# Performance work log

Measured on AMD Instinct MI355X. Metric: run time of the kernel, lower is better.

## Reference

```python
import jax, jax.numpy as jnp
import numpy as np
import math

E = 8          # num_experts
IN = 1024      # input_size
HID = 512      # head_size (expert hidden)
TOP_K = 2
B, P = 8, 1024


def setup_inputs() -> dict:
    key = jax.random.key(0)
    k1, k2, k3, k4, k5 = jax.random.split(key, 5)
    # expert weights init like ParallelExperts.reset_parameters (uniform xavier-ish)
    std1 = math.sqrt(2.0 / (IN + HID)); a1 = math.sqrt(3.0) * std1
    std2 = math.sqrt(2.0 / (HID + IN)); a2 = math.sqrt(3.0) * std2
    return {
        "x": jax.random.normal(k1, (B, P, IN), dtype=jnp.float32),
        "Q_isp": jax.random.normal(k2, (B, P, 1, IN), dtype=jnp.float32),
        "K_isp": jax.random.normal(k3, (B, P, E, IN), dtype=jnp.float32),
        "w1": jax.random.uniform(k4, (E, IN, HID), minval=-a1, maxval=a1, dtype=jnp.float32),
        "w2": jax.random.uniform(k5, (E, HID, IN), minval=-a2, maxval=a2, dtype=jnp.float32),
    }


def _gates(Q_isp, K_isp):
    # attention-based gating, eval path (no noise)
    N = K_isp.shape[2]
    scale = 1.0 / math.sqrt(K_isp.shape[-1])
    # [B,P,1,N] -> [T,N]
    scores = jnp.einsum('bpqd,bpnd->bpqn', Q_isp, K_isp)[:, :, 0, :].reshape(-1, N) * scale
    logits = jnp.nan_to_num(scores, nan=0.0, posinf=20.0, neginf=-20.0)
    probs = jax.nn.softmax(logits, axis=1)
    top_g, top_i = jax.lax.top_k(probs, TOP_K)
    # renormalize top-k gates; denominator detached as in torch (.detach())
    top_g = top_g / jax.lax.stop_gradient(top_g.sum(axis=1, keepdims=True) + 1e-6)
    T = probs.shape[0]
    gates = jnp.zeros_like(probs).at[jnp.arange(T)[:, None], top_i].set(top_g)
    return gates  # [T, E]


def reference(x, Q_isp, K_isp, w1, w2):
    gates = _gates(Q_isp, K_isp)                       # [T,E]
    T = gates.shape[0]
    xt = x.reshape(T, -1)                              # [T,IN]
    # grouped expert GEMMs (dense-masked form; gates are 0 off top-k)
    h = jax.nn.gelu(jnp.einsum('ti,eio->teo', xt, w1), approximate=False)  # [T,E,HID]
    y = jnp.einsum('teo,eoi->tei', h, w2)              # [T,E,IN]
    out = jnp.einsum('tei,te->ti', y, gates)           # combine with gates
    return out.reshape(x.shape)
```

## Files before the change

### kernel.cpp

```cpp
#include <hip/hip_runtime.h>
#include <math.h>

#define TT 8192
#define NE 8
#define DIN 1024
#define DH 512

typedef __attribute__((ext_vector_type(8))) short short8;
typedef __attribute__((ext_vector_type(4))) float f32x4;
typedef __attribute__((ext_vector_type(4))) unsigned short us4;

static const size_t OFF_CNT    = 0;
static const size_t OFF_BASE   = 256;
static const size_t OFF_TOKEXP = 512;
static const size_t OFF_GPAIR  = OFF_TOKEXP + (size_t)TT * 8;
static const size_t OFF_SLOT0  = OFF_GPAIR  + (size_t)TT * 8;
static const size_t OFF_SLOT1  = OFF_SLOT0  + (size_t)TT * 4;
static const size_t OFF_TOK    = OFF_SLOT1  + (size_t)TT * 4;
static const size_t OFF_GATE   = OFF_TOK    + (size_t)NE * TT * 4;
static const size_t OFF_XB     = OFF_GATE   + (size_t)NE * TT * 4;
static const size_t OFF_W1T    = OFF_XB     + (size_t)TT * DIN * 2;
static const size_t OFF_W2T    = OFF_W1T    + (size_t)NE * DH * DIN * 2;
static const size_t OFF_H      = OFF_W2T    + (size_t)NE * DIN * DH * 2;
static const size_t OFF_Y      = OFF_H      + (size_t)2 * TT * DH * 2;

__device__ __forceinline__ unsigned short f2bf(float f) {
    union { float f; unsigned u; } v; v.f = f;
    unsigned r = (v.u + 0x7fffu + ((v.u >> 16) & 1u)) >> 16;
    return (unsigned short)r;
}
__device__ __forceinline__ float bf2f(unsigned short u) {
    union { unsigned u; float f; } v; v.u = ((unsigned)u) << 16;
    return v.f;
}
__device__ __forceinline__ void async_copy16(const void* g, void* l) {
    __builtin_amdgcn_global_load_lds(
        (const __attribute__((address_space(1))) void*)g,
        (__attribute__((address_space(3))) void*)l, 16, 0, 0);
}

__global__ __launch_bounds__(256) void convert_x_kernel(const float* __restrict__ x,
                                                        unsigned short* __restrict__ xb)
{
    size_t i = ((size_t)blockIdx.x * 256 + threadIdx.x) * 8;
    float4 a = *reinterpret_cast<const float4*>(x + i);
    float4 b = *reinterpret_cast<const float4*>(x + i + 4);
    us4 o0 = { f2bf(a.x), f2bf(a.y), f2bf(a.z), f2bf(a.w) };
    us4 o1 = { f2bf(b.x), f2bf(b.y), f2bf(b.z), f2bf(b.w) };
    *reinterpret_cast<us4*>(xb + i)     = o0;
    *reinterpret_cast<us4*>(xb + i + 4) = o1;
}

__global__ __launch_bounds__(256) void convert_w_kernel(const float* __restrict__ src,
                                                        unsigned short* __restrict__ dst,
                                                        int K, int N)
{
    int e = blockIdx.z;
    int k0 = blockIdx.x * 32, n0 = blockIdx.y * 32;
    __shared__ float tile[32][33];
    int tx = threadIdx.x & 31, ty = threadIdx.x >> 5;
    const float* s = src + ((size_t)e * K + k0) * N + n0;
#pragma unroll
    for (int r = 0; r < 32; r += 8) tile[ty + r][tx] = s[(size_t)(ty + r) * N + tx];
    __syncthreads();
    unsigned short* d = dst + ((size_t)e * N + n0) * K + k0;
#pragma unroll
    for (int r = 0; r < 32; r += 8) d[(size_t)(ty + r) * K + tx] = f2bf(tile[tx][ty + r]);
}

__global__ __launch_bounds__(256) void gate_kernel(
    const float* __restrict__ Q, const float* __restrict__ Kc,
    int2* __restrict__ tokexp, float2* __restrict__ gpair)
{
    int wave = threadIdx.x >> 6, lane = threadIdx.x & 63;
    int t = blockIdx.x * 4 + wave;
    const float4* q4 = reinterpret_cast<const float4*>(Q + (size_t)t * DIN);
    const float4* k4 = reinterpret_cast<const float4*>(Kc + (size_t)t * NE * DIN);
    float4 q[4];
#pragma unroll
    for (int j = 0; j < 4; ++j) q[j] = q4[j * 64 + lane];
    float part[NE];
#pragma unroll
    for (int e = 0; e < NE; ++e) {
        float s = 0.0f;
#pragma unroll
        for (int j = 0; j < 4; ++j) {
            float4 kv = k4[e * 256 + j * 64 + lane];
            s += q[j].x * kv.x + q[j].y * kv.y + q[j].z * kv.z + q[j].w * kv.w;
        }
        part[e] = s;
    }
#pragma unroll
    for (int e = 0; e < NE; ++e) {
#pragma unroll
        for (int m = 1; m < 64; m <<= 1) part[e] += __shfl_xor(part[e], m);
    }
    if (lane == 0) {
        float s[NE];
#pragma unroll
        for (int e = 0; e < NE; ++e) {
            float v = part[e] * 0.03125f;
            if (isnan(v)) v = 0.0f;
            else if (isinf(v)) v = (v > 0.0f) ? 20.0f : -20.0f;
            s[e] = v;
        }
        float m = s[0];
        for (int e = 1; e < NE; ++e) m = fmaxf(m, s[e]);
        float p[NE]; float sum = 0.0f;
        for (int e = 0; e < NE; ++e) { p[e] = expf(s[e] - m); sum += p[e]; }
        float inv = 1.0f / sum;
        for (int e = 0; e < NE; ++e) p[e] *= inv;
        int i0 = 0;
        for (int e = 1; e < NE; ++e) if (p[e] > p[i0]) i0 = e;
        int i1 = (i0 == 0) ? 1 : 0;
        for (int e = 0; e < NE; ++e) if (e != i0 && p[e] > p[i1]) i1 = e;
        float denom = p[i0] + p[i1] + 1e-6f;
        tokexp[t] = make_int2(i0, i1);
        gpair[t]  = make_float2(p[i0] / denom, p[i1] / denom);
    }
}

__global__ __launch_bounds__(1024) void count_kernel(const int2* __restrict__ tokexp,
                                                     int* __restrict__ cnt)
{
    int e = blockIdx.x;
    int tid = threadIdx.x;
    int local = 0;
#pragma unroll
    for (int r = 0; r < TT / 1024; ++r) {
        int2 te = tokexp[r * 1024 + tid];
        local += (te.x == e || te.y == e) ? 1 : 0;
    }
#pragma unroll
    for (int m = 1; m < 64; m <<= 1) local += __shfl_xor(local, m);
    __shared__ int wsum[16];
    int wave = tid >> 6, lane = tid & 63;
    if (lane == 0) wsum[wave] = local;
    __syncthreads();
    if (tid == 0) {
        int s = 0;
        for (int w = 0; w < 16; ++w) s += wsum[w];
        cnt[e] = s;
    }
}

__global__ void scan_kernel(const int* __restrict__ cnt, int* __restrict__ base)
{
    if (threadIdx.x == 0) {
        int s = 0;
        for (int e = 0; e < NE; ++e) { base[e] = s; s += cnt[e]; }
    }
}

__global__ __launch_bounds__(1024) void build_kernel(
    const int2* __restrict__ tokexp, const float2* __restrict__ gpair,
    const int* __restrict__ base,
    int* __restrict__ tok_list, float* __restrict__ gate_list,
    int* __restrict__ slot0, int* __restrict__ slot1)
{
    int e = blockIdx.x;
    int tid = threadIdx.x;
    int wave = tid >> 6, lane = tid & 63;
    __shared__ int wsum[16];
    __shared__ int running;
    if (tid == 0) running = base[e];
    __syncthreads();
    int eb = base[e];
#pragma unroll 1
    for (int r = 0; r < TT / 1024; ++r) {
        int t = r * 1024 + tid;
        int2 te = tokexp[t];
        float2 g = gpair[t];
        bool f0 = (te.x == e), f1 = (te.y == e);
        bool f = f0 || f1;
        unsigned long long mask = __ballot(f);
        int mypos = __popcll(mask & ((1ull << lane) - 1ull));
        if (lane == 0) wsum[wave] = __popcll(mask);
        __syncthreads();
        int off = 0, total = 0;
        for (int w = 0; w < 16; ++w) {
            int c = wsum[w];
            if (w < wave) off += c;
            total += c;
        }
        int pos = running + off + mypos;
        if (f) {
            int j = pos - eb;
            tok_list[e * TT + j]  = t;
            gate_list[e * TT + j] = f0 ? g.x : g.y;
            if (f0) slot0[t] = pos; else slot1[t] = pos;
        }
        __syncthreads();
        if (tid == 0) running += total;
        __syncthreads();
    }
}

__global__ __launch_bounds__(256) void gemm1_kernel(
    const unsigned short* __restrict__ xb, const unsigned short* __restrict__ w1t,
    const int* __restrict__ cnt, const int* __restrict__ base,
    const int* __restrict__ tok_list, unsigned short* __restrict__ h)
{
    int e = blockIdx.z;
    int Te = cnt[e];
    int m0 = blockIdx.x * 128;
    if (m0 >= Te) return;
    int n0 = blockIdx.y * 128;

    __shared__ __align__(16) char smem[16384];
    __shared__ int rows[128];
    char* As = smem;
    char* Bs = smem + 8192;

    int tid = threadIdx.x;
    if (tid < 128) rows[tid] = (m0 + tid < Te) ? tok_list[e * TT + m0 + tid] : 0;
    __syncthreads();

    int w = tid >> 6, lane = tid & 63;
    int wm = w & 1, wn = w >> 1;
    int mcol = lane & 15;
    int kq = (lane >> 4) * 8;

    const unsigned short* w1e = w1t + (size_t)e * DH * DIN;
    const unsigned short* pa0 = xb + (size_t)rows[(2 * w + 0) * 16 + mcol] * DIN + kq;
    const unsigned short* pa1 = xb + (size_t)rows[(2 * w + 1) * 16 + mcol] * DIN + kq;
    const unsigned short* pb0 = w1e + (size_t)(n0 + (2 * w + 0) * 16 + mcol) * DIN + kq;
    const unsigned short* pb1 = w1e + (size_t)(n0 + (2 * w + 1) * 16 + mcol) * DIN + kq;
    char* dA0 = As + (2 * w + 0) * 1024;
    char* dA1 = As + (2 * w + 1) * 1024;
    char* dB0 = Bs + (2 * w + 0) * 1024;
    char* dB1 = Bs + (2 * w + 1) * 1024;

    f32x4 acc[4][4];
#pragma unroll
    for (int i = 0; i < 4; i++)
#pragma unroll
        for (int j = 0; j < 4; j++) acc[i][j] = {0.f, 0.f, 0.f, 0.f};

    for (int k0 = 0; k0 < DIN; k0 += 32) {
        __syncthreads();
        async_copy16(pa0, dA0); async_copy16(pa1, dA1);
        async_copy16(pb0, dB0); async_copy16(pb1, dB1);
        pa0 += 32; pa1 += 32; pb0 += 32; pb1 += 32;
        __syncthreads();
        short8 af[4], bfr[4];
#pragma unroll
        for (int mt = 0; mt < 4; ++mt)
            af[mt] = *reinterpret_cast<const short8*>(As + (wm * 4 + mt) * 1024 + lane * 16);
#pragma unroll
        for (int nt = 0; nt < 4; ++nt)
            bfr[nt] = *reinterpret_cast<const short8*>(Bs + (wn * 4 + nt) * 1024 + lane * 16);
#pragma unroll
        for (int mt = 0; mt < 4; ++mt)
#pragma unroll
            for (int nt = 0; nt < 4; ++nt)
                acc[mt][nt] = __builtin_amdgcn_mfma_f32_16x16x32_bf16(af[mt], bfr[nt], acc[mt][nt], 0, 0, 0);
    }

    int hb = base[e] + m0;
#pragma unroll
    for (int mt = 0; mt < 4; ++mt) {
        int rbase = (wm * 4 + mt) * 16 + ((lane >> 4) * 4);
#pragma unroll
        for (int r = 0; r < 4; ++r) {
            int row = rbase + r;
            if (m0 + row < Te) {
#pragma unroll
                for (int nt = 0; nt < 4; ++nt) {
                    float u = acc[mt][nt][r];
                    float g = 0.5f * u * (1.0f + erff(u * 0.70710678118f));
                    int col = n0 + (wn * 4 + nt) * 16 + mcol;
                    h[(size_t)(hb + row) * DH + col] = f2bf(g);
                }
            }
        }
    }
}

__global__ __launch_bounds__(256) void gemm2_kernel(
    const unsigned short* __restrict__ h, const unsigned short* __restrict__ w2t,
    const int* __restrict__ cnt, const int* __restrict__ base,
    const float* __restrict__ gate_list, unsigned short* __restrict__ y)
{
    int e = blockIdx.z;
    int Te = cnt[e];
    int m0 = blockIdx.x * 128;
    if (m0 >= Te) return;
    int n0 = blockIdx.y * 128;

    __shared__ __align__(16) char smem[16384];
    __shared__ float gts[128];
    char* As = smem;
    char* Bs = smem + 8192;

    int tid = threadIdx.x;
    if (tid < 128) gts[tid] = (m0 + tid < Te) ? gate_list[e * TT + m0 + tid] : 0.0f;

    int w = tid >> 6, lane = tid & 63;
    int wm = w & 1, wn = w >> 1;
    int mcol = lane & 15;
    int kq = (lane >> 4) * 8;
    int hb = base[e];

    int r0 = m0 + (2 * w + 0) * 16 + mcol; if (r0 >= Te) r0 = Te - 1;
    int r1 = m0 + (2 * w + 1) * 16 + mcol; if (r1 >= Te) r1 = Te - 1;
    const unsigned short* w2e = w2t + (size_t)e * DIN * DH;
    const unsigned short* pa0 = h + (size_t)(hb + r0) * DH + kq;
    const unsigned short* pa1 = h + (size_t)(hb + r1) * DH + kq;
    const unsigned short* pb0 = w2e + (size_t)(n0 + (2 * w + 0) * 16 + mcol) * DH + kq;
    const unsigned short* pb1 = w2e + (size_t)(n0 + (2 * w + 1) * 16 + mcol) * DH + kq;
    char* dA0 = As + (2 * w + 0) * 1024;
    char* dA1 = As + (2 * w + 1) * 1024;
    char* dB0 = Bs + (2 * w + 0) * 1024;
    char* dB1 = Bs + (2 * w + 1) * 1024;

    f32x4 acc[4][4];
#pragma unroll
    for (int i = 0; i < 4; i++)
#pragma unroll
        for (int j = 0; j < 4; j++) acc[i][j] = {0.f, 0.f, 0.f, 0.f};

    for (int k0 = 0; k0 < DH; k0 += 32) {
        __syncthreads();
        async_copy16(pa0, dA0); async_copy16(pa1, dA1);
        async_copy16(pb0, dB0); async_copy16(pb1, dB1);
        pa0 += 32; pa1 += 32; pb0 += 32; pb1 += 32;
        __syncthreads();
        short8 af[4], bfr[4];
#pragma unroll
        for (int mt = 0; mt < 4; ++mt)
            af[mt] = *reinterpret_cast<const short8*>(As + (wm * 4 + mt) * 1024 + lane * 16);
#pragma unroll
        for (int nt = 0; nt < 4; ++nt)
            bfr[nt] = *reinterpret_cast<const short8*>(Bs + (wn * 4 + nt) * 1024 + lane * 16);
#pragma unroll
        for (int mt = 0; mt < 4; ++mt)
#pragma unroll
            for (int nt = 0; nt < 4; ++nt)
                acc[mt][nt] = __builtin_amdgcn_mfma_f32_16x16x32_bf16(af[mt], bfr[nt], acc[mt][nt], 0, 0, 0);
    }

#pragma unroll
    for (int mt = 0; mt < 4; ++mt) {
        int rbase = (wm * 4 + mt) * 16 + ((lane >> 4) * 4);
#pragma unroll
        for (int r = 0; r < 4; ++r) {
            int row = rbase + r;
            if (m0 + row < Te) {
                float g = gts[row];
#pragma unroll
                for (int nt = 0; nt < 4; ++nt) {
                    int col = n0 + (wn * 4 + nt) * 16 + mcol;
                    y[(size_t)(hb + m0 + row) * DIN + col] = f2bf(acc[mt][nt][r] * g);
                }
            }
        }
    }
}

__global__ __launch_bounds__(256) void combine_kernel(
    const unsigned short* __restrict__ y,
    const int* __restrict__ slot0, const int* __restrict__ slot1,
    float* __restrict__ out)
{
    int t = blockIdx.x;
    int c = threadIdx.x * 4;
    const unsigned short* y0 = y + (size_t)slot0[t] * DIN + c;
    const unsigned short* y1 = y + (size_t)slot1[t] * DIN + c;
    us4 u0 = *reinterpret_cast<const us4*>(y0);
    us4 u1 = *reinterpret_cast<const us4*>(y1);
    float4 o;
    o.x = bf2f(u0.x) + bf2f(u1.x);
    o.y = bf2f(u0.y) + bf2f(u1.y);
    o.z = bf2f(u0.z) + bf2f(u1.z);
    o.w = bf2f(u0.w) + bf2f(u1.w);
    *reinterpret_cast<float4*>(out + (size_t)t * DIN + c) = o;
}

extern "C" void kernel_launch(void* const* d_in, const int* in_sizes, int n_in,
                              void* d_out, int out_size, void* d_ws, size_t ws_size,
                              hipStream_t stream) {
    const float* x  = (const float*)d_in[0];
    const float* Q  = (const float*)d_in[1];
    const float* K  = (const float*)d_in[2];
    const float* w1 = (const float*)d_in[3];
    const float* w2 = (const float*)d_in[4];
    float* out = (float*)d_out;

    char* ws = (char*)d_ws;
    int*    cnt       = (int*)(ws + OFF_CNT);
    int*    base      = (int*)(ws + OFF_BASE);
    int2*   tokexp    = (int2*)(ws + OFF_TOKEXP);
    float2* gpair     = (float2*)(ws + OFF_GPAIR);
    int*    slot0     = (int*)(ws + OFF_SLOT0);
    int*    slot1     = (int*)(ws + OFF_SLOT1);
    int*    tok_list  = (int*)(ws + OFF_TOK);
    float*  gate_list = (float*)(ws + OFF_GATE);
    unsigned short* xb  = (unsigned short*)(ws + OFF_XB);
    unsigned short* w1t = (unsigned short*)(ws + OFF_W1T);
    unsigned short* w2t = (unsigned short*)(ws + OFF_W2T);
    unsigned short* h   = (unsigned short*)(ws + OFF_H);
    unsigned short* y   = (unsigned short*)(ws + OFF_Y);

    convert_x_kernel<<<TT * DIN / (256 * 8), 256, 0, stream>>>(x, xb);
    convert_w_kernel<<<dim3(DIN / 32, DH / 32, NE), 256, 0, stream>>>(w1, w1t, DIN, DH);
    convert_w_kernel<<<dim3(DH / 32, DIN / 32, NE), 256, 0, stream>>>(w2, w2t, DH, DIN);
    gate_kernel<<<TT / 4, 256, 0, stream>>>(Q, K, tokexp, gpair);
    count_kernel<<<NE, 1024, 0, stream>>>(tokexp, cnt);
    scan_kernel<<<1, 64, 0, stream>>>(cnt, base);
    build_kernel<<<NE, 1024, 0, stream>>>(tokexp, gpair, base, tok_list, gate_list, slot0, slot1);
    gemm1_kernel<<<dim3(TT / 128, DH / 128, NE), 256, 0, stream>>>(xb, w1t, cnt, base, tok_list, h);
    gemm2_kernel<<<dim3(TT / 128, DIN / 128, NE), 256, 0, stream>>>(h, w2t, cnt, base, gate_list, y);
    combine_kernel<<<TT, 256, 0, stream>>>(y, slot0, slot1, out);
}
```

Baseline: 627.3 us.

## Fuse prep kernels, merge routing, double-buffer GEMM K loops, fast GELU

Merges the x/weight conversion and gating kernels into one launch, and folds count, scan and build into a single routing kernel that builds a shared histogram. Both expert GEMMs now take 64-wide K steps with double-buffered LDS (64KB per block), so the next tile's async loads overlap the current MFMAs with one barrier per step. erff is replaced by a polynomial erf approximation, and combine handles four tokens per block. The larger LDS footprint may lower occupancy, and the GELU approximation adds a small numeric error.

```diff
diff --git a/kernel.cpp b/kernel.cpp
--- a/kernel.cpp
+++ b/kernel.cpp
@@ -39,133 +39,147 @@
         (__attribute__((address_space(3))) void*)l, 16, 0, 0);
 }
 
-__global__ __launch_bounds__(256) void convert_x_kernel(const float* __restrict__ x,
-                                                        unsigned short* __restrict__ xb)
-{
-    size_t i = ((size_t)blockIdx.x * 256 + threadIdx.x) * 8;
-    float4 a = *reinterpret_cast<const float4*>(x + i);
-    float4 b = *reinterpret_cast<const float4*>(x + i + 4);
-    us4 o0 = { f2bf(a.x), f2bf(a.y), f2bf(a.z), f2bf(a.w) };
-    us4 o1 = { f2bf(b.x), f2bf(b.y), f2bf(b.z), f2bf(b.w) };
-    *reinterpret_cast<us4*>(xb + i)     = o0;
-    *reinterpret_cast<us4*>(xb + i + 4) = o1;
-}
-
-__global__ __launch_bounds__(256) void convert_w_kernel(const float* __restrict__ src,
-                                                        unsigned short* __restrict__ dst,
-                                                        int K, int N)
-{
-    int e = blockIdx.z;
-    int k0 = blockIdx.x * 32, n0 = blockIdx.y * 32;
-    __shared__ float tile[32][33];
-    int tx = threadIdx.x & 31, ty = threadIdx.x >> 5;
-    const float* s = src + ((size_t)e * K + k0) * N + n0;
-#pragma unroll
-    for (int r = 0; r < 32; r += 8) tile[ty + r][tx] = s[(size_t)(ty + r) * N + tx];
-    __syncthreads();
-    unsigned short* d = dst + ((size_t)e * N + n0) * K + k0;
-#pragma unroll
-    for (int r = 0; r < 32; r += 8) d[(size_t)(ty + r) * K + tx] = f2bf(tile[tx][ty + r]);
-}
-
-__global__ __launch_bounds__(256) void gate_kernel(
+__device__ __forceinline__ float gelu_erf(float u) {
+    float z  = 0.70710678118f * u;
+    float az = fabsf(z);
+    float t  = __builtin_amdgcn_rcpf(__builtin_fmaf(0.3275911f, az, 1.0f));
+    float p  = t * (0.254829592f + t * (-0.284496736f + t * (1.421413741f +
+               t * (-1.453152027f + t * 1.061405429f))));
+    float e2 = exp2f(-1.4426950408889634f * az * az);
+    float er = __builtin_fmaf(-p, e2, 1.0f);
+    er = copysignf(er, z);
+    return 0.5f * u * (1.0f + er);
+}
+
+__global__ __launch_bounds__(256) void prep_kernel(
+    const float* __restrict__ x, const float* __restrict__ w1, const float* __restrict__ w2,
     const float* __restrict__ Q, const float* __restrict__ Kc,
+    unsigned short* __restrict__ xb, unsigned short* __restrict__ w1t,
+    unsigned short* __restrict__ w2t,
     int2* __restrict__ tokexp, float2* __restrict__ gpair)
 {
-    int wave = threadIdx.x >> 6, lane = threadIdx.x & 63;
-    int t = blockIdx.x * 4 + wave;
-    const float4* q4 = reinterpret_cast<const float4*>(Q + (size_t)t * DIN);
-    const float4* k4 = reinterpret_cast<const float4*>(Kc + (size_t)t * NE * DIN);
-    float4 q[4];
-#pragma unroll
-    for (int j = 0; j < 4; ++j) q[j] = q4[j * 64 + lane];
-    float part[NE];
-#pragma unroll
-    for (int e = 0; e < NE; ++e) {
-        float s = 0.0f;
-#pragma unroll
-        for (int j = 0; j < 4; ++j) {
-            float4 kv = k4[e * 256 + j * 64 + lane];
-            s += q[j].x * kv.x + q[j].y * kv.y + q[j].z * kv.z + q[j].w * kv.w;
-        }
-        part[e] = s;
-    }
-#pragma unroll
-    for (int e = 0; e < NE; ++e) {
-#pragma unroll
-        for (int m = 1; m < 64; m <<= 1) part[e] += __shfl_xor(part[e], m);
-    }
-    if (lane == 0) {
-        float s[NE];
+    __shared__ float tile[32][33];
+    int bid = blockIdx.x;
+    int tid = threadIdx.x;
+
+    if (bid < 4096) {
+        size_t i = ((size_t)bid * 256 + tid) * 8;
+        float4 a = *reinterpret_cast<const float4*>(x + i);
+        float4 b = *reinterpret_cast<const float4*>(x + i + 4);
+        us4 o0 = { f2bf(a.x), f2bf(a.y), f2bf(a.z), f2bf(a.w) };
+        us4 o1 = { f2bf(b.x), f2bf(b.y), f2bf(b.z), f2bf(b.w) };
+        *reinterpret_cast<us4*>(xb + i)     = o0;
+        *reinterpret_cast<us4*>(xb + i + 4) = o1;
+    } else if (bid < 12288) {
+        const float* src; unsigned short* dst; int K, N, e, k0, n0;
+        if (bid < 8192) {
+            int r = bid - 4096; e = r >> 9; int rem = r & 511;
+            k0 = (rem & 31) * 32; n0 = (rem >> 5) * 32;
+            src = w1; dst = w1t; K = DIN; N = DH;
+        } else {
+            int r = bid - 8192; e = r >> 9; int rem = r & 511;
+            k0 = (rem & 15) * 32; n0 = (rem >> 4) * 32;
+            src = w2; dst = w2t; K = DH; N = DIN;
+        }
+        int tx = tid & 31, ty = tid >> 5;
+        const float* s = src + ((size_t)e * K + k0) * N + n0;
+#pragma unroll
+        for (int r2 = 0; r2 < 32; r2 += 8) tile[ty + r2][tx] = s[(size_t)(ty + r2) * N + tx];
+        __syncthreads();
+        unsigned short* d = dst + ((size_t)e * N + n0) * K + k0;
+#pragma unroll
+        for (int r2 = 0; r2 < 32; r2 += 8) d[(size_t)(ty + r2) * K + tx] = f2bf(tile[tx][ty + r2]);
+    } else {
+        int wave = tid >> 6, lane = tid & 63;
+        int t = (bid - 12288) * 4 + wave;
+        const float4* q4 = reinterpret_cast<const float4*>(Q + (size_t)t * DIN);
+        const float4* k4 = reinterpret_cast<const float4*>(Kc + (size_t)t * NE * DIN);
+        float4 q[4];
+#pragma unroll
+        for (int j = 0; j < 4; ++j) q[j] = q4[j * 64 + lane];
+        float part[NE];
 #pragma unroll
         for (int e = 0; e < NE; ++e) {
-            float v = part[e] * 0.03125f;
-            if (isnan(v)) v = 0.0f;
-            else if (isinf(v)) v = (v > 0.0f) ? 20.0f : -20.0f;
-            s[e] = v;
-        }
-        float m = s[0];
-        for (int e = 1; e < NE; ++e) m = fmaxf(m, s[e]);
-        float p[NE]; float sum = 0.0f;
-        for (int e = 0; e < NE; ++e) { p[e] = expf(s[e] - m); sum += p[e]; }
-        float inv = 1.0f / sum;
-        for (int e = 0; e < NE; ++e) p[e] *= inv;
-        int i0 = 0;
-        for (int e = 1; e < NE; ++e) if (p[e] > p[i0]) i0 = e;
-        int i1 = (i0 == 0) ? 1 : 0;
-        for (int e = 0; e < NE; ++e) if (e != i0 && p[e] > p[i1]) i1 = e;
-        float denom = p[i0] + p[i1] + 1e-6f;
-        tokexp[t] = make_int2(i0, i1);
-        gpair[t]  = make_float2(p[i0] / denom, p[i1] / denom);
-    }
-}
-
-__global__ __launch_bounds__(1024) void count_kernel(const int2* __restrict__ tokexp,
-                                                     int* __restrict__ cnt)
-{
-    int e = blockIdx.x;
-    int tid = threadIdx.x;
-    int local = 0;
-#pragma unroll
-    for (int r = 0; r < TT / 1024; ++r) {
-        int2 te = tokexp[r * 1024 + tid];
-        local += (te.x == e || te.y == e) ? 1 : 0;
-    }
-#pragma unroll
-    for (int m = 1; m < 64; m <<= 1) local += __shfl_xor(local, m);
-    __shared__ int wsum[16];
-    int wave = tid >> 6, lane = tid & 63;
-    if (lane == 0) wsum[wave] = local;
-    __syncthreads();
-    if (tid == 0) {
-        int s = 0;
-        for (int w = 0; w < 16; ++w) s += wsum[w];
-        cnt[e] = s;
-    }
-}
-
-__global__ void scan_kernel(const int* __restrict__ cnt, int* __restrict__ base)
-{
-    if (threadIdx.x == 0) {
-        int s = 0;
-        for (int e = 0; e < NE; ++e) { base[e] = s; s += cnt[e]; }
-    }
-}
-
-__global__ __launch_bounds__(1024) void build_kernel(
+            float s = 0.0f;
+#pragma unroll
+            for (int j = 0; j < 4; ++j) {
+                float4 kv = k4[e * 256 + j * 64 + lane];
+                s += q[j].x * kv.x + q[j].y * kv.y + q[j].z * kv.z + q[j].w * kv.w;
+            }
+            part[e] = s;
+        }
+#pragma unroll
+        for (int e = 0; e < NE; ++e) {
+#pragma unroll
+            for (int m = 1; m < 64; m <<= 1) part[e] += __shfl_xor(part[e], m);
+        }
+        if (lane == 0) {
+            float s[NE];
+#pragma unroll
+            for (int e = 0; e < NE; ++e) {
+                float v = part[e] * 0.03125f;
+                if (isnan(v)) v = 0.0f;
+                else if (isinf(v)) v = (v > 0.0f) ? 20.0f : -20.0f;
+                s[e] = v;
+            }
+            float m = s[0];
+            for (int e = 1; e < NE; ++e) m = fmaxf(m, s[e]);
+            float p[NE]; float sum = 0.0f;
+            for (int e = 0; e < NE; ++e) { p[e] = expf(s[e] - m); sum += p[e]; }
+            float inv = 1.0f / sum;
+            for (int e = 0; e < NE; ++e) p[e] *= inv;
+            int i0 = 0;
+            for (int e = 1; e < NE; ++e) if (p[e] > p[i0]) i0 = e;
+            int i1 = (i0 == 0) ? 1 : 0;
+            for (int e = 0; e < NE; ++e) if (e != i0 && p[e] > p[i1]) i1 = e;
+            float denom = p[i0] + p[i1] + 1e-6f;
+            tokexp[t] = make_int2(i0, i1);
+            gpair[t]  = make_float2(p[i0] / denom, p[i1] / denom);
+        }
+    }
+}
+
+__global__ __launch_bounds__(1024) void route_kernel(
     const int2* __restrict__ tokexp, const float2* __restrict__ gpair,
-    const int* __restrict__ base,
+    int* __restrict__ cnt, int* __restrict__ base,
     int* __restrict__ tok_list, float* __restrict__ gate_list,
     int* __restrict__ slot0, int* __restrict__ slot1)
 {
     int e = blockIdx.x;
     int tid = threadIdx.x;
     int wave = tid >> 6, lane = tid & 63;
+    __shared__ int hist[NE];
     __shared__ int wsum[16];
     __shared__ int running;
-    if (tid == 0) running = base[e];
+
+    if (tid < NE) hist[tid] = 0;
     __syncthreads();
-    int eb = base[e];
+
+    int lc[NE];
+#pragma unroll
+    for (int j = 0; j < NE; ++j) lc[j] = 0;
+#pragma unroll
+    for (int r = 0; r < TT / 1024; ++r) {
+        int2 te = tokexp[r * 1024 + tid];
+#pragma unroll
+        for (int j = 0; j < NE; ++j) lc[j] += (te.x == j ? 1 : 0) + (te.y == j ? 1 : 0);
+    }
+#pragma unroll
+    for (int j = 0; j < NE; ++j) {
+        int v = lc[j];
+#pragma unroll
+        for (int m = 1; m < 64; m <<= 1) v += __shfl_xor(v, m);
+        if (lane == 0) atomicAdd(&hist[j], v);
+    }
+    __syncthreads();
+
+    int b = 0;
+#pragma unroll
+    for (int j = 0; j < NE; ++j) if (j < e) b += hist[j];
+    if (tid == 0) { cnt[e] = hist[e]; base[e] = b; running = b; }
+    __syncthreads();
+
+    int eb = b;
 #pragma unroll 1
     for (int r = 0; r < TT / 1024; ++r) {
         int t = r * 1024 + tid;
@@ -207,29 +221,38 @@
     if (m0 >= Te) return;
     int n0 = blockIdx.y * 128;
 
-    __shared__ __align__(16) char smem[16384];
-    __shared__ int rows[128];
-    char* As = smem;
-    char* Bs = smem + 8192;
+    __shared__ __align__(16) char smem[65536];
 
     int tid = threadIdx.x;
-    if (tid < 128) rows[tid] = (m0 + tid < Te) ? tok_list[e * TT + m0 + tid] : 0;
-    __syncthreads();
-
     int w = tid >> 6, lane = tid & 63;
     int wm = w & 1, wn = w >> 1;
     int mcol = lane & 15;
     int kq = (lane >> 4) * 8;
 
+    int ia0 = m0 + (2 * w + 0) * 16 + mcol;
+    int ia1 = m0 + (2 * w + 1) * 16 + mcol;
+    int ra0 = (ia0 < Te) ? tok_list[e * TT + ia0] : 0;
+    int ra1 = (ia1 < Te) ? tok_list[e * TT + ia1] : 0;
+
     const unsigned short* w1e = w1t + (size_t)e * DH * DIN;
-    const unsigned short* pa0 = xb + (size_t)rows[(2 * w + 0) * 16 + mcol] * DIN + kq;
-    const unsigned short* pa1 = xb + (size_t)rows[(2 * w + 1) * 16 + mcol] * DIN + kq;
+    const unsigned short* pa0 = xb + (size_t)ra0 * DIN + kq;
+    const unsigned short* pa1 = xb + (size_t)ra1 * DIN + kq;
     const unsigned short* pb0 = w1e + (size_t)(n0 + (2 * w + 0) * 16 + mcol) * DIN + kq;
     const unsigned short* pb1 = w1e + (size_t)(n0 + (2 * w + 1) * 16 + mcol) * DIN + kq;
-    char* dA0 = As + (2 * w + 0) * 1024;
-    char* dA1 = As + (2 * w + 1) * 1024;
-    char* dB0 = Bs + (2 * w + 0) * 1024;
-    char* dB1 = Bs + (2 * w + 1) * 1024;
+
+    int d0 = (2 * w + 0) * 1024;
+    int d1 = (2 * w + 1) * 1024;
+
+#define STAGE1(buf, koff) do { \
+    async_copy16(pa0 + (koff),      (buf) + d0); \
+    async_copy16(pa1 + (koff),      (buf) + d1); \
+    async_copy16(pa0 + (koff) + 32, (buf) + 8192  + d0); \
+    async_copy16(pa1 + (koff) + 32, (buf) + 8192  + d1); \
+    async_copy16(pb0 + (koff),      (buf) + 16384 + d0); \
+    async_copy16(pb1 + (koff),      (buf) + 16384 + d1); \
+    async_copy16(pb0 + (koff) + 32, (buf) + 24576 + d0); \
+    async_copy16(pb1 + (koff) + 32, (buf) + 24576 + d1); \
+} while (0)
 
     f32x4 acc[4][4];
 #pragma unroll
@@ -237,25 +260,35 @@
 #pragma unroll
         for (int j = 0; j < 4; j++) acc[i][j] = {0.f, 0.f, 0.f, 0.f};
 
-    for (int k0 = 0; k0 < DIN; k0 += 32) {
-        __syncthreads();
-        async_copy16(pa0, dA0); async_copy16(pa1, dA1);
-        async_copy16(pb0, dB0); async_copy16(pb1, dB1);
-        pa0 += 32; pa1 += 32; pb0 += 32; pb1 += 32;
-        __syncthreads();
-        short8 af[4], bfr[4];
-#pragma unroll
-        for (int mt = 0; mt < 4; ++mt)
-            af[mt] = *reinterpret_cast<const short8*>(As + (wm * 4 + mt) * 1024 + lane * 16);
-#pragma unroll
-        for (int nt = 0; nt < 4; ++nt)
-            bfr[nt] = *reinterpret_cast<const short8*>(Bs + (wn * 4 + nt) * 1024 + lane * 16);
-#pragma unroll
-        for (int mt = 0; mt < 4; ++mt)
+    char* cur = smem;
+    char* nxt = smem + 32768;
+
+    STAGE1(cur, 0);
+    __syncthreads();
+
+    const int NT = DIN / 64;
+    for (int t = 0; t < NT; ++t) {
+        if (t + 1 < NT) STAGE1(nxt, (t + 1) * 64);
+#pragma unroll
+        for (int half = 0; half < 2; ++half) {
+            const char* cb = cur + half * 8192;
+            short8 af[4], bfr[4];
+#pragma unroll
+            for (int mt = 0; mt < 4; ++mt)
+                af[mt] = *reinterpret_cast<const short8*>(cb + (wm * 4 + mt) * 1024 + lane * 16);
 #pragma unroll
             for (int nt = 0; nt < 4; ++nt)
-                acc[mt][nt] = __builtin_amdgcn_mfma_f32_16x16x32_bf16(af[mt], bfr[nt], acc[mt][nt], 0, 0, 0);
-    }
+                bfr[nt] = *reinterpret_cast<const short8*>(cb + 16384 + (wn * 4 + nt) * 1024 + lane * 16);
+#pragma unroll
+            for (int mt = 0; mt < 4; ++mt)
+#pragma unroll
+                for (int nt = 0; nt < 4; ++nt)
+                    acc[mt][nt] = __builtin_amdgcn_mfma_f32_16x16x32_bf16(af[mt], bfr[nt], acc[mt][nt], 0, 0, 0);
+        }
+        __syncthreads();
+        char* tmp = cur; cur = nxt; nxt = tmp;
+    }
+#undef STAGE1
 
     int hb = base[e] + m0;
 #pragma unroll
@@ -267,8 +300,7 @@
             if (m0 + row < Te) {
 #pragma unroll
                 for (int nt = 0; nt < 4; ++nt) {
-                    float u = acc[mt][nt][r];
-                    float g = 0.5f * u * (1.0f + erff(u * 0.70710678118f));
+                    float g = gelu_erf(acc[mt][nt][r]);
                     int col = n0 + (wn * 4 + nt) * 16 + mcol;
                     h[(size_t)(hb + row) * DH + col] = f2bf(g);
                 }
@@ -288,14 +320,9 @@
     if (m0 >= Te) return;
     int n0 = blockIdx.y * 128;
 
-    __shared__ __align__(16) char smem[16384];
-    __shared__ float gts[128];
-    char* As = smem;
-    char* Bs = smem + 8192;
+    __shared__ __align__(16) char smem[65536];
 
     int tid = threadIdx.x;
-    if (tid < 128) gts[tid] = (m0 + tid < Te) ? gate_list[e * TT + m0 + tid] : 0.0f;
-
     int w = tid >> 6, lane = tid & 63;
     int wm = w & 1, wn = w >> 1;
     int mcol = lane & 15;
@@ -309,10 +336,20 @@
     const unsigned short* pa1 = h + (size_t)(hb + r1) * DH + kq;
     const unsigned short* pb0 = w2e + (size_t)(n0 + (2 * w + 0) * 16 + mcol) * DH + kq;
     const unsigned short* pb1 = w2e + (size_t)(n0 + (2 * w + 1) * 16 + mcol) * DH + kq;
-    char* dA0 = As + (2 * w + 0) * 1024;
-    char* dA1 = As + (2 * w + 1) * 1024;
-    char* dB0 = Bs + (2 * w + 0) * 1024;
-    char* dB1 = Bs + (2 * w + 1) * 1024;
+
+    int d0 = (2 * w + 0) * 1024;
+    int d1 = (2 * w + 1) * 1024;
+
+#define STAGE2(buf, koff) do { \
+    async_copy16(pa0 + (koff),      (buf) + d0); \
+    async_copy16(pa1 + (koff),      (buf) + d1); \
+    async_copy16(pa0 + (koff) + 32, (buf) + 8192  + d0); \
+    async_copy16(pa1 + (koff) + 32, (buf) + 8192  + d1); \
+    async_copy16(pb0 + (koff),      (buf) + 16384 + d0); \
+    async_copy16(pb1 + (koff),      (buf) + 16384 + d1); \
+    async_copy16(pb0 + (koff) + 32, (buf) + 24576 + d0); \
+    async_copy16(pb1 + (koff) + 32, (buf) + 24576 + d1); \
+} while (0)
 
     f32x4 acc[4][4];
 #pragma unroll
@@ -320,25 +357,35 @@
 #pragma unroll
         for (int j = 0; j < 4; j++) acc[i][j] = {0.f, 0.f, 0.f, 0.f};
 
-    for (int k0 = 0; k0 < DH; k0 += 32) {
-        __syncthreads();
-        async_copy16(pa0, dA0); async_copy16(pa1, dA1);
-        async_copy16(pb0, dB0); async_copy16(pb1, dB1);
-        pa0 += 32; pa1 += 32; pb0 += 32; pb1 += 32;
-        __syncthreads();
-        short8 af[4], bfr[4];
-#pragma unroll
-        for (int mt = 0; mt < 4; ++mt)
-            af[mt] = *reinterpret_cast<const short8*>(As + (wm * 4 + mt) * 1024 + lane * 16);
-#pragma unroll
-        for (int nt = 0; nt < 4; ++nt)
-            bfr[nt] = *reinterpret_cast<const short8*>(Bs + (wn * 4 + nt) * 1024 + lane * 16);
-#pragma unroll
-        for (int mt = 0; mt < 4; ++mt)
+    char* cur = smem;
+    char* nxt = smem + 32768;
+
+    STAGE2(cur, 0);
+    __syncthreads();
+
+    const int NT = DH / 64;
+    for (int t = 0; t < NT; ++t) {
+        if (t + 1 < NT) STAGE2(nxt, (t + 1) * 64);
+#pragma unroll
+        for (int half = 0; half < 2; ++half) {
+            const char* cb = cur + half * 8192;
+            short8 af[4], bfr[4];
+#pragma unroll
+            for (int mt = 0; mt < 4; ++mt)
+                af[mt] = *reinterpret_cast<const short8*>(cb + (wm * 4 + mt) * 1024 + lane * 16);
 #pragma unroll
             for (int nt = 0; nt < 4; ++nt)
-                acc[mt][nt] = __builtin_amdgcn_mfma_f32_16x16x32_bf16(af[mt], bfr[nt], acc[mt][nt], 0, 0, 0);
-    }
+                bfr[nt] = *reinterpret_cast<const short8*>(cb + 16384 + (wn * 4 + nt) * 1024 + lane * 16);
+#pragma unroll
+            for (int mt = 0; mt < 4; ++mt)
+#pragma unroll
+                for (int nt = 0; nt < 4; ++nt)
+                    acc[mt][nt] = __builtin_amdgcn_mfma_f32_16x16x32_bf16(af[mt], bfr[nt], acc[mt][nt], 0, 0, 0);
+        }
+        __syncthreads();
+        char* tmp = cur; cur = nxt; nxt = tmp;
+    }
+#undef STAGE2
 
 #pragma unroll
     for (int mt = 0; mt < 4; ++mt) {
@@ -347,7 +394,7 @@
         for (int r = 0; r < 4; ++r) {
             int row = rbase + r;
             if (m0 + row < Te) {
-                float g = gts[row];
+                float g = gate_list[e * TT + m0 + row];
 #pragma unroll
                 for (int nt = 0; nt < 4; ++nt) {
                     int col = n0 + (wn * 4 + nt) * 16 + mcol;
@@ -363,18 +410,21 @@
     const int* __restrict__ slot0, const int* __restrict__ slot1,
     float* __restrict__ out)
 {
-    int t = blockIdx.x;
     int c = threadIdx.x * 4;
-    const unsigned short* y0 = y + (size_t)slot0[t] * DIN + c;
-    const unsigned short* y1 = y + (size_t)slot1[t] * DIN + c;
-    us4 u0 = *reinterpret_cast<const us4*>(y0);
-    us4 u1 = *reinterpret_cast<const us4*>(y1);
-    float4 o;
-    o.x = bf2f(u0.x) + bf2f(u1.x);
-    o.y = bf2f(u0.y) + bf2f(u1.y);
-    o.z = bf2f(u0.z) + bf2f(u1.z);
-    o.w = bf2f(u0.w) + bf2f(u1.w);
-    *reinterpret_cast<float4*>(out + (size_t)t * DIN + c) = o;
+#pragma unroll
+    for (int r = 0; r < 4; ++r) {
+        int t = blockIdx.x * 4 + r;
+        const unsigned short* y0 = y + (size_t)slot0[t] * DIN + c;
+        const unsigned short* y1 = y + (size_t)slot1[t] * DIN + c;
+        us4 u0 = *reinterpret_cast<const us4*>(y0);
+        us4 u1 = *reinterpret_cast<const us4*>(y1);
+        float4 o;
+        o.x = bf2f(u0.x) + bf2f(u1.x);
+        o.y = bf2f(u0.y) + bf2f(u1.y);
+        o.z = bf2f(u0.z) + bf2f(u1.z);
+        o.w = bf2f(u0.w) + bf2f(u1.w);
+        *reinterpret_cast<float4*>(out + (size_t)t * DIN + c) = o;
+    }
 }
 
 extern "C" void kernel_launch(void* const* d_in, const int* in_sizes, int n_in,
@@ -402,14 +452,10 @@
     unsigned short* h   = (unsigned short*)(ws + OFF_H);
     unsigned short* y   = (unsigned short*)(ws + OFF_Y);
 
-    convert_x_kernel<<<TT * DIN / (256 * 8), 256, 0, stream>>>(x, xb);
-    convert_w_kernel<<<dim3(DIN / 32, DH / 32, NE), 256, 0, stream>>>(w1, w1t, DIN, DH);
-    convert_w_kernel<<<dim3(DH / 32, DIN / 32, NE), 256, 0, stream>>>(w2, w2t, DH, DIN);
-    gate_kernel<<<TT / 4, 256, 0, stream>>>(Q, K, tokexp, gpair);
-    count_kernel<<<NE, 1024, 0, stream>>>(tokexp, cnt);
-    scan_kernel<<<1, 64, 0, stream>>>(cnt, base);
-    build_kernel<<<NE, 1024, 0, stream>>>(tokexp, gpair, base, tok_list, gate_list, slot0, slot1);
+    prep_kernel<<<14336, 256, 0, stream>>>(x, w1, w2, Q, K, xb, w1t, w2t, tokexp, gpair);
+    route_kernel<<<NE, 1024, 0, stream>>>(tokexp, gpair, cnt, base,
+                                          tok_list, gate_list, slot0, slot1);
     gemm1_kernel<<<dim3(TT / 128, DH / 128, NE), 256, 0, stream>>>(xb, w1t, cnt, base, tok_list, h);
     gemm2_kernel<<<dim3(TT / 128, DIN / 128, NE), 256, 0, stream>>>(h, w2t, cnt, base, gate_list, y);
-    combine_kernel<<<TT, 256, 0, stream>>>(y, slot0, slot1, out);
-}
+    combine_kernel<<<TT / 4, 256, 0, stream>>>(y, slot0, slot1, out);
+}
```

After: 610.1 us. 1.03x faster.
